# Performance work log

Hardware: AMD Instinct MI355X
Metric: run time of the kernel (lower is better)

Reference implementation:

```python
import jax, jax.numpy as jnp
import numpy as np

COMMIT_W = 0.25
ENT_W = 0.1
ENT_T = 0.01
EPS = 1e-5


def setup_inputs() -> dict:
    key = jax.random.key(0)
    kx, kc = jax.random.split(key)
    x = jax.random.normal(kx, (32, 32, 32, 256), dtype=jnp.float32)
    # variance_scaling(1.0, fan_in, uniform) -> U(-sqrt(3/fan_in), sqrt(3/fan_in)), fan_in = 256
    lim = float(np.sqrt(3.0 / 256.0))
    codebook = jax.random.uniform(kc, (1024, 256), dtype=jnp.float32, minval=-lim, maxval=lim)
    return {"x": x, "codebook": codebook}


def _cdist(flat, codebook):
    # Euclidean distance (with sqrt, as jnp.linalg.norm in the original),
    # computed via the expanded quadratic form to avoid the [N,K,D] intermediate.
    d2 = (jnp.sum(flat * flat, axis=-1, keepdims=True)
          + jnp.sum(codebook * codebook, axis=-1)[None, :]
          - 2.0 * (flat @ codebook.T))
    return jnp.sqrt(jnp.maximum(d2, 0.0))  # [N, K]


def reference(x, codebook):
    D = x.shape[-1]
    flat = x.reshape(-1, D)                      # [N, D]
    distances = _cdist(flat, codebook)           # [N, K]
    flat_indices = jnp.argmin(distances, axis=-1)  # [N]
    indices = flat_indices.reshape(x.shape[:-1])
    # one_hot(indices) @ codebook == gather
    quantized = codebook[flat_indices].reshape(x.shape)

    # optax.l2_loss = 0.5 * (pred - target)^2
    commit_loss = 0.5 * jnp.mean((x - jax.lax.stop_gradient(quantized)) ** 2) * COMMIT_W
    codebook_loss = 0.5 * jnp.mean((jax.lax.stop_gradient(x) - quantized) ** 2)

    # entropy loss on affinity = -distances
    logits = (-distances) / ENT_T                # [N, K]
    probs = jax.nn.softmax(logits, axis=-1)
    log_probs = jax.nn.log_softmax(logits + EPS, axis=-1)
    avg_probs = jnp.mean(probs, axis=0)          # [K]
    avg_entropy = -jnp.sum(avg_probs * jnp.log(avg_probs + EPS))
    sample_entropy = -jnp.mean(jnp.sum(probs * log_probs, axis=-1))
    entropy_loss = (sample_entropy - avg_entropy) * ENT_W

    vq_loss = codebook_loss + commit_loss + entropy_loss
    # straight-through estimator
    quantized_st = x + jax.lax.stop_gradient(quantized - x)
    return quantized_st, vq_loss, commit_loss, codebook_loss, entropy_loss, indices
```

## Files before the change

kernel.cpp:

```cpp
#include <hip/hip_runtime.h>

#define N_ROWS 32768
#define DIMS 256
#define K_CODES 1024
#define MT 32
#define NCHUNK 128
#define KC 32

static constexpr size_t SC_OFF  = 8388608;
static constexpr size_t IDX_OFF = 8388612;

__device__ inline float wsum64(float v){
  #pragma unroll
  for(int off=32; off; off>>=1) v += __shfl_xor(v, off, 64);
  return v;
}

__global__ __launch_bounds__(256) void rowsq_np512_kernel(const float* __restrict__ X,
                                                          const float* __restrict__ CB,
                                                          float* __restrict__ xsq,
                                                          float* __restrict__ csq){
  int r = blockIdx.x*256 + threadIdx.x;
  if(r >= K_CODES + N_ROWS) return;
  const float* src; float* dst;
  if(r < K_CODES){ src = CB + (size_t)r*DIMS; dst = csq + r; }
  else { src = X + (size_t)(r - K_CODES)*DIMS; dst = xsq + (r - K_CODES); }

  float blk[2];
  #pragma unroll
  for(int bb=0; bb<2; bb++){
    const float* s = src + bb*128;
    float q[128];
    #pragma unroll
    for(int i=0;i<32;i++){
      float4 v = *(const float4*)(s + i*4);
      q[i*4+0]=__fmul_rn(v.x,v.x); q[i*4+1]=__fmul_rn(v.y,v.y);
      q[i*4+2]=__fmul_rn(v.z,v.z); q[i*4+3]=__fmul_rn(v.w,v.w);
    }
    float v16[16];
    #pragma unroll
    for(int l=0;l<16;l++)
      v16[l] = __fadd_rn(__fadd_rn(__fadd_rn(q[l],     q[l+16]),
                                   __fadd_rn(q[l+32],  q[l+48])),
                         __fadd_rn(__fadd_rn(q[l+64],  q[l+80]),
                                   __fadd_rn(q[l+96],  q[l+112])));
    float w8[8];
    #pragma unroll
    for(int l=0;l<8;l++) w8[l] = __fadd_rn(v16[l], v16[l+8]);
    float u4[4];
    #pragma unroll
    for(int l=0;l<4;l++) u4[l] = __fadd_rn(w8[l], w8[l+4]);
    float t0 = __fadd_rn(u4[0], u4[2]);
    float t1 = __fadd_rn(u4[1], u4[3]);
    blk[bb] = __fadd_rn(t0, t1);
  }
  *dst = __fadd_rn(blk[0], blk[1]);
}

__global__ __launch_bounds__(256,4) void fused_argmin_kernel(
    const float* __restrict__ X, const float* __restrict__ CB,
    const float* __restrict__ xsq, const float* __restrict__ csq,
    float* __restrict__ hist, float* __restrict__ acc_sc,
    float* __restrict__ out)
{
  __shared__ float As[KC][34];
  __shared__ float Bs[KC][NCHUNK];
  __shared__ int   sk[MT];
  const int t  = threadIdx.x;
  const int tx = t & 15, ty = t >> 4;
  const int m0 = blockIdx.x * MT;

  float dm[2]; int km[2]; float Ss[2], Ts[2];

  const float xs0 = xsq[m0 + ty*2];
  const float xs1 = xsq[m0 + ty*2 + 1];

  const int arow = t >> 3;
  const int acol = (t & 7) * 4;
  const float* Ag = X + (size_t)(m0 + arow)*DIMS + acol;
  const int brow = t >> 1;
  const int bcol = (t & 1) * 16;

  float4 a4 = *(const float4*)(Ag);
  float4 b4[4];
  {
    const float* Bg0 = CB + (size_t)brow*DIMS + bcol;
    #pragma unroll
    for(int q=0;q<4;q++) b4[q] = *(const float4*)(Bg0 + q*4);
  }

  for(int nc=0; nc<8; nc++){
    const int n0c = nc*NCHUNK;
    const float* Bg = CB + (size_t)(n0c + brow)*DIMS + bcol;
    float acc[2][8];
    #pragma unroll
    for(int i=0;i<2;i++)
      #pragma unroll
      for(int j=0;j<8;j++) acc[i][j]=0.f;

    for(int kc=0;kc<8;kc++){
      __syncthreads();
      As[acol+0][arow]=a4.x; As[acol+1][arow]=a4.y;
      As[acol+2][arow]=a4.z; As[acol+3][arow]=a4.w;
      #pragma unroll
      for(int q=0;q<4;q++){
        Bs[bcol+q*4+0][brow]=b4[q].x; Bs[bcol+q*4+1][brow]=b4[q].y;
        Bs[bcol+q*4+2][brow]=b4[q].z; Bs[bcol+q*4+3][brow]=b4[q].w;
      }
      __syncthreads();
      {
        const float* An = Ag + ((kc+1)&7)*KC;
        const float* Bn = (kc < 7) ? (Bg + (kc+1)*KC)
                                   : (CB + (size_t)((((nc+1)&7)*NCHUNK) + brow)*DIMS + bcol);
        a4 = *(const float4*)An;
        #pragma unroll
        for(int q=0;q<4;q++) b4[q] = *(const float4*)(Bn + q*4);
      }
      #pragma unroll
      for(int k=0;k<KC;k++){
        float2 a2 = *(const float2*)&As[k][ty*2];
        float4 b0 = *(const float4*)&Bs[k][tx*4];
        float4 b1 = *(const float4*)&Bs[k][64 + tx*4];
        float bv[8]={b0.x,b0.y,b0.z,b0.w,b1.x,b1.y,b1.z,b1.w};
        #pragma unroll
        for(int j=0;j<8;j++){
          acc[0][j] = fmaf(a2.x, bv[j], acc[0][j]);
          acc[1][j] = fmaf(a2.y, bv[j], acc[1][j]);
        }
      }
    }

    float csv[8];
    { float4 c0 = *(const float4*)(csq + n0c + tx*4);
      float4 c1 = *(const float4*)(csq + n0c + 64 + tx*4);
      csv[0]=c0.x; csv[1]=c0.y; csv[2]=c0.z; csv[3]=c0.w;
      csv[4]=c1.x; csv[5]=c1.y; csv[6]=c1.z; csv[7]=c1.w; }
    #pragma unroll
    for(int i=0;i<2;i++){
      float xs = i ? xs1 : xs0;
      float d[8];
      #pragma unroll
      for(int j=0;j<8;j++){
        float d2 = (xs + csv[j]) - 2.0f*acc[i][j];
        d[j] = sqrtf(fmaxf(d2, 0.f));
      }
      float dl = INFINITY; int kl = 0;
      #pragma unroll
      for(int j=0;j<8;j++){
        int kidx = n0c + (j>>2)*64 + tx*4 + (j&3);
        if(d[j] < dl){ dl = d[j]; kl = kidx; }
      }
      #pragma unroll
      for(int off=1; off<16; off<<=1){
        float od = __shfl_xor(dl, off, 64);
        int   ok = __shfl_xor(kl, off, 64);
        if(od < dl || (od == dl && ok < kl)){ dl = od; kl = ok; }
      }
      float s1=0.f, t2s=0.f;
      #pragma unroll
      for(int j=0;j<8;j++){
        float l = (dl - d[j])*100.0f;
        float e = expf(l);
        s1 += e; t2s = fmaf(e, l, t2s);
      }
      #pragma unroll
      for(int off=1; off<16; off<<=1){
        s1  += __shfl_xor(s1,  off, 64);
        t2s += __shfl_xor(t2s, off, 64);
      }
      if(nc == 0){
        dm[i]=dl; km[i]=kl; Ss[i]=s1; Ts[i]=t2s;
      } else {
        if(dl < dm[i]){
          float del = 100.0f*(dl - dm[i]); float al = expf(del);
          Ts[i] = al*(Ts[i] + Ss[i]*del) + t2s;
          Ss[i] = al*Ss[i] + s1;
          dm[i] = dl; km[i] = kl;
        } else {
          float del = 100.0f*(dm[i] - dl); float al = expf(del);
          Ts[i] += al*(t2s + s1*del);
          Ss[i] += al*s1;
        }
      }
    }
  }

  float plogp = 0.f;
  if(tx == 0){
    #pragma unroll
    for(int i=0;i<2;i++){
      int n = m0 + ty*2 + i;
      out[IDX_OFF + n] = (float)km[i];
      sk[ty*2 + i] = km[i];
      atomicAdd(hist + km[i], 1.0f);
      plogp += Ts[i]/Ss[i] - logf(Ss[i]);
    }
  }
  plogp = wsum64(plogp);
  if((t & 63) == 0) atomicAdd(acc_sc + 1, plogp);

  __syncthreads();
  {
    int w = t>>6, lane = t&63;
    int row0 = w*8;
    float mse = 0.f;
    #pragma unroll
    for(int r=0;r<8;r++){
      int n = m0 + row0 + r;
      int k = sk[row0 + r];
      float4 cb4 = *(const float4*)(CB + (size_t)k*DIMS + lane*4);
      float4 x4  = *(const float4*)(X  + (size_t)n*DIMS + lane*4);
      float e0=x4.x-cb4.x, e1=x4.y-cb4.y, e2=x4.z-cb4.z, e3=x4.w-cb4.w;
      mse += e0*e0 + e1*e1 + e2*e2 + e3*e3;
      *reinterpret_cast<float4*>(out + (size_t)n*DIMS + lane*4) = cb4;
    }
    mse = wsum64(mse);
    if(lane==0) atomicAdd(acc_sc+0, mse);
  }
}

__global__ __launch_bounds__(256) void finalize_kernel(const float* __restrict__ hist,
                                                       const float* __restrict__ acc_sc,
                                                       float* __restrict__ out){
  __shared__ float red[256];
  int t = threadIdx.x;
  float s = 0.f;
  #pragma unroll
  for(int c=0;c<4;c++){
    float ap = hist[c*256 + t] * (1.0f/32768.0f);
    s += ap * logf(ap + 1e-5f);
  }
  red[t] = s; __syncthreads();
  for(int off=128; off; off>>=1){
    if(t<off) red[t]+=red[t+off];
    __syncthreads();
  }
  if(t==0){
    float avg_entropy    = -red[0];
    float mse            = acc_sc[0] * (1.0f/8388608.0f);
    float sample_entropy = -(acc_sc[1] * (1.0f/32768.0f));
    float commit = 0.5f*mse*0.25f;
    float cbl    = 0.5f*mse;
    float ent    = (sample_entropy - avg_entropy)*0.1f;
    float vq     = cbl + commit + ent;
    out[SC_OFF+0] = vq;
    out[SC_OFF+1] = commit;
    out[SC_OFF+2] = cbl;
    out[SC_OFF+3] = ent;
  }
}

extern "C" void kernel_launch(void* const* d_in, const int* in_sizes, int n_in,
                              void* d_out, int out_size, void* d_ws, size_t ws_size,
                              hipStream_t stream){
  const float* X  = (const float*)d_in[0];
  const float* CB = (const float*)d_in[1];
  float* out = (float*)d_out;
  float* xsq     = (float*)d_ws + N_ROWS;
  float* csq     = xsq + N_ROWS;
  float* hist    = csq + K_CODES;
  float* acc_sc  = hist + K_CODES;

  hipMemsetAsync(hist, 0, (K_CODES+2)*sizeof(float), stream);
  rowsq_np512_kernel <<<(K_CODES+N_ROWS+255)/256, 256, 0, stream>>>(X, CB, xsq, csq);
  fused_argmin_kernel<<<N_ROWS/MT, 256, 0, stream>>>(X, CB, xsq, csq, hist, acc_sc, out);
  finalize_kernel    <<<1, 256, 0, stream>>>(hist, acc_sc, out);
}
```

Baseline: 450.5 us.

## Enlarge argmin GEMM tile to 64x256 with 4x16 register blocking

Doubles the rows per block (64) and the codes per chunk (256), so each thread computes a 4x16 accumulator tile instead of 2x8. The aim is more FMAs per shared-memory load and fewer passes over the codebook per block. The shared-memory strides are padded to reduce bank conflicts, and the staging loads are rearranged so each thread loads one codebook row segment. The cost is much higher register pressure (64 accumulators plus 40 prefetch registers) and a launch bound lowered to 2 blocks, which reduces occupancy and halves the grid size.

```diff
diff --git a/kernel.cpp b/kernel.cpp
--- a/kernel.cpp
+++ b/kernel.cpp
@@ -3,9 +3,11 @@
 #define N_ROWS 32768
 #define DIMS 256
 #define K_CODES 1024
-#define MT 32
-#define NCHUNK 128
+#define MT 64
+#define NCHUNK 256
 #define KC 32
+#define SA 68
+#define SB 260
 
 static constexpr size_t SC_OFF  = 8388608;
 static constexpr size_t IDX_OFF = 8388612;
@@ -57,96 +59,103 @@
   *dst = __fadd_rn(blk[0], blk[1]);
 }
 
-__global__ __launch_bounds__(256,4) void fused_argmin_kernel(
+__global__ __launch_bounds__(256,2) void fused_argmin_kernel(
     const float* __restrict__ X, const float* __restrict__ CB,
     const float* __restrict__ xsq, const float* __restrict__ csq,
     float* __restrict__ hist, float* __restrict__ acc_sc,
     float* __restrict__ out)
 {
-  __shared__ float As[KC][34];
-  __shared__ float Bs[KC][NCHUNK];
+  __shared__ float As[KC][SA];
+  __shared__ float Bs[KC][SB];
   __shared__ int   sk[MT];
   const int t  = threadIdx.x;
   const int tx = t & 15, ty = t >> 4;
   const int m0 = blockIdx.x * MT;
 
-  float dm[2]; int km[2]; float Ss[2], Ts[2];
-
-  const float xs0 = xsq[m0 + ty*2];
-  const float xs1 = xsq[m0 + ty*2 + 1];
-
-  const int arow = t >> 3;
-  const int acol = (t & 7) * 4;
+  float dm[4]; int km[4]; float Ss[4], Ts[4];
+
+  float4 xs4 = *(const float4*)(xsq + m0 + ty*4);
+  float xs_[4] = {xs4.x, xs4.y, xs4.z, xs4.w};
+
+  const int arow = t >> 2;
+  const int acol = (t & 3) * 8;
   const float* Ag = X + (size_t)(m0 + arow)*DIMS + acol;
-  const int brow = t >> 1;
-  const int bcol = (t & 1) * 16;
-
-  float4 a4 = *(const float4*)(Ag);
-  float4 b4[4];
+
+  float4 a4p[2], b4p[8];
+  a4p[0] = *(const float4*)(Ag);
+  a4p[1] = *(const float4*)(Ag + 4);
   {
-    const float* Bg0 = CB + (size_t)brow*DIMS + bcol;
-    #pragma unroll
-    for(int q=0;q<4;q++) b4[q] = *(const float4*)(Bg0 + q*4);
-  }
-
-  for(int nc=0; nc<8; nc++){
+    const float* Bg = CB + (size_t)t*DIMS;
+    #pragma unroll
+    for(int q=0;q<8;q++) b4p[q] = *(const float4*)(Bg + q*4);
+  }
+
+  for(int nc=0; nc<4; nc++){
     const int n0c = nc*NCHUNK;
-    const float* Bg = CB + (size_t)(n0c + brow)*DIMS + bcol;
-    float acc[2][8];
-    #pragma unroll
-    for(int i=0;i<2;i++)
-      #pragma unroll
-      for(int j=0;j<8;j++) acc[i][j]=0.f;
+    float acc[4][16];
+    #pragma unroll
+    for(int i=0;i<4;i++)
+      #pragma unroll
+      for(int j=0;j<16;j++) acc[i][j]=0.f;
 
     for(int kc=0;kc<8;kc++){
       __syncthreads();
-      As[acol+0][arow]=a4.x; As[acol+1][arow]=a4.y;
-      As[acol+2][arow]=a4.z; As[acol+3][arow]=a4.w;
-      #pragma unroll
-      for(int q=0;q<4;q++){
-        Bs[bcol+q*4+0][brow]=b4[q].x; Bs[bcol+q*4+1][brow]=b4[q].y;
-        Bs[bcol+q*4+2][brow]=b4[q].z; Bs[bcol+q*4+3][brow]=b4[q].w;
+      #pragma unroll
+      for(int q=0;q<2;q++){
+        As[acol+q*4+0][arow]=a4p[q].x; As[acol+q*4+1][arow]=a4p[q].y;
+        As[acol+q*4+2][arow]=a4p[q].z; As[acol+q*4+3][arow]=a4p[q].w;
+      }
+      #pragma unroll
+      for(int q=0;q<8;q++){
+        Bs[q*4+0][t]=b4p[q].x; Bs[q*4+1][t]=b4p[q].y;
+        Bs[q*4+2][t]=b4p[q].z; Bs[q*4+3][t]=b4p[q].w;
       }
       __syncthreads();
       {
-        const float* An = Ag + ((kc+1)&7)*KC;
-        const float* Bn = (kc < 7) ? (Bg + (kc+1)*KC)
-                                   : (CB + (size_t)((((nc+1)&7)*NCHUNK) + brow)*DIMS + bcol);
-        a4 = *(const float4*)An;
+        int nkc = kc+1, nnc = nc;
+        if(nkc==8){ nkc=0; nnc=(nc+1)&3; }
+        const float* An = Ag + nkc*KC;
+        const float* Bn = CB + (size_t)(nnc*NCHUNK + t)*DIMS + nkc*KC;
+        a4p[0]=*(const float4*)(An); a4p[1]=*(const float4*)(An+4);
         #pragma unroll
-        for(int q=0;q<4;q++) b4[q] = *(const float4*)(Bn + q*4);
+        for(int q=0;q<8;q++) b4p[q]=*(const float4*)(Bn + q*4);
       }
       #pragma unroll
       for(int k=0;k<KC;k++){
-        float2 a2 = *(const float2*)&As[k][ty*2];
+        float4 av = *(const float4*)&As[k][ty*4];
         float4 b0 = *(const float4*)&Bs[k][tx*4];
-        float4 b1 = *(const float4*)&Bs[k][64 + tx*4];
-        float bv[8]={b0.x,b0.y,b0.z,b0.w,b1.x,b1.y,b1.z,b1.w};
+        float4 b1 = *(const float4*)&Bs[k][64  + tx*4];
+        float4 b2 = *(const float4*)&Bs[k][128 + tx*4];
+        float4 b3 = *(const float4*)&Bs[k][192 + tx*4];
+        float a_[4]={av.x,av.y,av.z,av.w};
+        float b_[16]={b0.x,b0.y,b0.z,b0.w, b1.x,b1.y,b1.z,b1.w,
+                      b2.x,b2.y,b2.z,b2.w, b3.x,b3.y,b3.z,b3.w};
         #pragma unroll
-        for(int j=0;j<8;j++){
-          acc[0][j] = fmaf(a2.x, bv[j], acc[0][j]);
-          acc[1][j] = fmaf(a2.y, bv[j], acc[1][j]);
-        }
-      }
-    }
-
-    float csv[8];
-    { float4 c0 = *(const float4*)(csq + n0c + tx*4);
-      float4 c1 = *(const float4*)(csq + n0c + 64 + tx*4);
-      csv[0]=c0.x; csv[1]=c0.y; csv[2]=c0.z; csv[3]=c0.w;
-      csv[4]=c1.x; csv[5]=c1.y; csv[6]=c1.z; csv[7]=c1.w; }
-    #pragma unroll
-    for(int i=0;i<2;i++){
-      float xs = i ? xs1 : xs0;
-      float d[8];
-      #pragma unroll
-      for(int j=0;j<8;j++){
+        for(int r=0;r<4;r++)
+          #pragma unroll
+          for(int j=0;j<16;j++)
+            acc[r][j] = fmaf(a_[r], b_[j], acc[r][j]);
+      }
+    }
+
+    float csv[16];
+    #pragma unroll
+    for(int g=0;g<4;g++){
+      float4 c4 = *(const float4*)(csq + n0c + g*64 + tx*4);
+      csv[g*4+0]=c4.x; csv[g*4+1]=c4.y; csv[g*4+2]=c4.z; csv[g*4+3]=c4.w;
+    }
+    #pragma unroll
+    for(int i=0;i<4;i++){
+      float xs = xs_[i];
+      float d[16];
+      #pragma unroll
+      for(int j=0;j<16;j++){
         float d2 = (xs + csv[j]) - 2.0f*acc[i][j];
         d[j] = sqrtf(fmaxf(d2, 0.f));
       }
       float dl = INFINITY; int kl = 0;
       #pragma unroll
-      for(int j=0;j<8;j++){
+      for(int j=0;j<16;j++){
         int kidx = n0c + (j>>2)*64 + tx*4 + (j&3);
         if(d[j] < dl){ dl = d[j]; kl = kidx; }
       }
@@ -158,7 +167,7 @@
       }
       float s1=0.f, t2s=0.f;
       #pragma unroll
-      for(int j=0;j<8;j++){
+      for(int j=0;j<16;j++){
         float l = (dl - d[j])*100.0f;
         float e = expf(l);
         s1 += e; t2s = fmaf(e, l, t2s);
@@ -188,10 +197,10 @@
   float plogp = 0.f;
   if(tx == 0){
     #pragma unroll
-    for(int i=0;i<2;i++){
-      int n = m0 + ty*2 + i;
+    for(int i=0;i<4;i++){
+      int n = m0 + ty*4 + i;
       out[IDX_OFF + n] = (float)km[i];
-      sk[ty*2 + i] = km[i];
+      sk[ty*4 + i] = km[i];
       atomicAdd(hist + km[i], 1.0f);
       plogp += Ts[i]/Ss[i] - logf(Ss[i]);
     }
@@ -202,10 +211,10 @@
   __syncthreads();
   {
     int w = t>>6, lane = t&63;
-    int row0 = w*8;
+    int row0 = w*16;
     float mse = 0.f;
     #pragma unroll
-    for(int r=0;r<8;r++){
+    for(int r=0;r<16;r++){
       int n = m0 + row0 + r;
       int k = sk[row0 + r];
       float4 cb4 = *(const float4*)(CB + (size_t)k*DIMS + lane*4);
```

Measured after the change: 393.3 us. 12.7% less time.
